# Performance work log

Hardware: AMD Instinct MI355X
Metric: run time of the kernel (lower is better)

The kernel has to match this reference:

```python
import jax, jax.numpy as jnp
import numpy as np

CUTOFF = 100.0
SR = 16000.0
Q = 0.7071067811865476  # 1/sqrt(2), torchaudio default
BATCH, T = 64, 480000


def _biquad_coeffs():
    # RBJ highpass biquad coefficients, normalized by a0
    w0 = 2.0 * np.pi * CUTOFF / SR
    alpha = np.sin(w0) / (2.0 * Q)
    cosw = np.cos(w0)
    b0 = (1.0 + cosw) / 2.0
    b1 = -(1.0 + cosw)
    b2 = b0
    a0 = 1.0 + alpha
    a1 = -2.0 * cosw
    a2 = 1.0 - alpha
    return tuple(float(c / a0) for c in (b0, b1, b2, a1, a2))


def setup_inputs() -> dict:
    key = jax.random.key(0)
    audio = jax.random.normal(key, (BATCH, T), dtype=jnp.float32)
    return {"audio": audio}


def reference(audio):
    # audio: [B, T]; order-2 IIR (Direct Form I) recurrence along time
    b0, b1, b2, a1, a2 = _biquad_coeffs()

    def step(carry, x):
        x1, x2, y1, y2 = carry  # each [B]
        y = b0 * x + b1 * x1 + b2 * x2 - a1 * y1 - a2 * y2
        return (x, x1, y, y1), y

    B = audio.shape[0]
    z = jnp.zeros((B,), audio.dtype)
    _, ys = jax.lax.scan(step, (z, z, z, z), audio.T)  # ys: [T, B]
    return ys.T
```

## Files before the change

kernel.cpp:

```cpp
#include <hip/hip_runtime.h>
#include <cmath>

#define T_LEN 480000
#define BATCH 64
#define CHUNK 128
#define WARM  320
#define NCH   ((T_LEN + CHUNK - 1) / CHUNK)
#define BLKS  32

#define STEP(xi, yo) do {                                   \
    float f_  = fmaf(b0, (xi), fmaf(b1, x1, b2 * x2));      \
    float g_  = fmaf(c2, y2, f_);                           \
    float yy_ = fmaf(c1, y1, g_);                           \
    x2 = x1; x1 = (xi);                                     \
    y2 = y1; y1 = yy_;                                      \
    (yo) = yy_;                                             \
} while (0)

__global__ __launch_bounds__(256) void highpass_kernel(
    const float* __restrict__ in, float* __restrict__ out,
    const float b0, const float b1, const float b2,
    const float c1, const float c2)
{
    const int idx = blockIdx.x * blockDim.x + threadIdx.x;
    if (idx >= BATCH * NCH) return;
    const int r = idx / NCH;
    const int c = idx - r * NCH;

    const size_t rowoff = (size_t)r * T_LEN;
    const int begin = c * CHUNK;
    int end = begin + CHUNK; if (end > T_LEN) end = T_LEN;
    int start = begin - WARM; if (start < 0) start = 0;

    const float4* __restrict__ xv = (const float4*)(in  + rowoff + start);
    float4*       __restrict__ yv = (float4*)      (out + rowoff + start);

    const int nblk = (end - start) / BLKS;
    const int wblk = (begin - start) / BLKS;

    float x1 = 0.f, x2 = 0.f, y1 = 0.f, y2 = 0.f;

    float4 cur[8], nxt[8];
#pragma unroll
    for (int i = 0; i < 8; ++i) cur[i] = xv[i];

    for (int b = 0; b < nblk; ++b) {
        if (b + 1 < nblk) {
#pragma unroll
            for (int i = 0; i < 8; ++i) nxt[i] = xv[(b + 1) * 8 + i];
        }

        float4 o[8];
#pragma unroll
        for (int i = 0; i < 8; ++i) {
            float4 v = cur[i];
            float4 q;
            STEP(v.x, q.x);
            STEP(v.y, q.y);
            STEP(v.z, q.z);
            STEP(v.w, q.w);
            o[i] = q;
        }

        if (b >= wblk) {
#pragma unroll
            for (int i = 0; i < 8; ++i) yv[b * 8 + i] = o[i];
        }

#pragma unroll
        for (int i = 0; i < 8; ++i) cur[i] = nxt[i];
    }
}

extern "C" void kernel_launch(void* const* d_in, const int* in_sizes, int n_in,
                              void* d_out, int out_size, void* d_ws, size_t ws_size,
                              hipStream_t stream) {
    const float* in  = (const float*)d_in[0];
    float*       out = (float*)d_out;

    const double Q     = 0.7071067811865476;
    const double w0    = 2.0 * M_PI * 100.0 / 16000.0;
    const double alpha = sin(w0) / (2.0 * Q);
    const double cosw  = cos(w0);
    const double b0d = (1.0 + cosw) / 2.0;
    const double b1d = -(1.0 + cosw);
    const double b2d = b0d;
    const double a0d = 1.0 + alpha;
    const double a1d = -2.0 * cosw;
    const double a2d = 1.0 - alpha;

    const float b0 = (float)(b0d / a0d);
    const float b1 = (float)(b1d / a0d);
    const float b2 = (float)(b2d / a0d);
    const float c1 = (float)(-(a1d / a0d));
    const float c2 = (float)(-(a2d / a0d));

    const int total  = BATCH * NCH;
    const int tblock = 256;
    const int grid   = (total + tblock - 1) / tblock;

    hipLaunchKernelGGL(highpass_kernel, dim3(grid), dim3(tblock), 0, stream,
                       in, out, b0, b1, b2, c1, c2);
}
```

Baseline: 267.0 us.

## Replace per-chunk warmup recurrence with block-level state propagation via matrix powers

Each thread now runs a short 64-sample chunk from zero output state. It publishes its end state to shared memory, then reconstructs its true initial state by combining the end states of the previous six threads through precomputed powers of the 2x2 feedback matrix (A^64 up to A^320). The old scheme had each thread recompute 320 warmup samples for only 128 outputs; this removes most of that redundant input reading and arithmetic. The cost is a second pass over the registers, a block barrier, and a truncated state history of about 384 samples, comparable to the previous warmup length.

```diff
diff --git a/kernel.cpp b/kernel.cpp
--- a/kernel.cpp
+++ b/kernel.cpp
@@ -3,10 +3,11 @@
 
 #define T_LEN 480000
 #define BATCH 64
-#define CHUNK 128
-#define WARM  320
-#define NCH   ((T_LEN + CHUNK - 1) / CHUNK)
-#define BLKS  32
+#define L     64
+#define WARMT 6
+#define OUTT  (256 - WARMT)
+#define SPB   (OUTT * L)
+#define BPR   (T_LEN / SPB)
 
 #define STEP(xi, yo) do {                                   \
     float f_  = fmaf(b0, (xi), fmaf(b1, x1, b2 * x2));      \
@@ -20,56 +21,78 @@
 __global__ __launch_bounds__(256) void highpass_kernel(
     const float* __restrict__ in, float* __restrict__ out,
     const float b0, const float b1, const float b2,
-    const float c1, const float c2)
+    const float c1, const float c2,
+    const float4 M1, const float4 M2, const float4 M3,
+    const float4 M4, const float4 M5)
 {
-    const int idx = blockIdx.x * blockDim.x + threadIdx.x;
-    if (idx >= BATCH * NCH) return;
-    const int r = idx / NCH;
-    const int c = idx - r * NCH;
+    const int r = blockIdx.x / BPR;
+    const int b = blockIdx.x - r * BPR;
+    const int t = threadIdx.x;
+    const size_t rowoff = (size_t)r * T_LEN;
+    const int start = b * SPB + (t - WARMT) * L;
 
-    const size_t rowoff = (size_t)r * T_LEN;
-    const int begin = c * CHUNK;
-    int end = begin + CHUNK; if (end > T_LEN) end = T_LEN;
-    int start = begin - WARM; if (start < 0) start = 0;
+    float4 v[16];
+    float pa = 0.f, pb = 0.f;
+    float xs1 = 0.f, xs2 = 0.f;
 
-    const float4* __restrict__ xv = (const float4*)(in  + rowoff + start);
-    float4*       __restrict__ yv = (float4*)      (out + rowoff + start);
+    const bool active = (start >= 0);
+    if (active) {
+        const float4* __restrict__ xv = (const float4*)(in + rowoff + start);
+#pragma unroll
+        for (int i = 0; i < 16; ++i) v[i] = xv[i];
+        if (start > 0) {
+            xs1 = in[rowoff + start - 1];
+            xs2 = in[rowoff + start - 2];
+        }
+        float x1 = xs1, x2 = xs2, y1 = 0.f, y2 = 0.f;
+#pragma unroll
+        for (int i = 0; i < 16; ++i) {
+            float d;
+            STEP(v[i].x, d); STEP(v[i].y, d); STEP(v[i].z, d); STEP(v[i].w, d);
+        }
+        pa = y1; pb = y2;
+    }
 
-    const int nblk = (end - start) / BLKS;
-    const int wblk = (begin - start) / BLKS;
+    __shared__ float2 pl[256];
+    pl[t] = make_float2(pa, pb);
+    __syncthreads();
+    if (t < WARMT) return;
 
-    float x1 = 0.f, x2 = 0.f, y1 = 0.f, y2 = 0.f;
+    const float2 q1 = pl[t - 1], q2 = pl[t - 2], q3 = pl[t - 3],
+                 q4 = pl[t - 4], q5 = pl[t - 5], q6 = pl[t - 6];
+    float Y1 = q1.x, Y2 = q1.y;
+    Y1 = fmaf(M1.x, q2.x, fmaf(M1.y, q2.y, Y1));
+    Y2 = fmaf(M1.z, q2.x, fmaf(M1.w, q2.y, Y2));
+    Y1 = fmaf(M2.x, q3.x, fmaf(M2.y, q3.y, Y1));
+    Y2 = fmaf(M2.z, q3.x, fmaf(M2.w, q3.y, Y2));
+    Y1 = fmaf(M3.x, q4.x, fmaf(M3.y, q4.y, Y1));
+    Y2 = fmaf(M3.z, q4.x, fmaf(M3.w, q4.y, Y2));
+    Y1 = fmaf(M4.x, q5.x, fmaf(M4.y, q5.y, Y1));
+    Y2 = fmaf(M4.z, q5.x, fmaf(M4.w, q5.y, Y2));
+    Y1 = fmaf(M5.x, q6.x, fmaf(M5.y, q6.y, Y1));
+    Y2 = fmaf(M5.z, q6.x, fmaf(M5.w, q6.y, Y2));
 
-    float4 cur[8], nxt[8];
+    {
+        float x1 = xs1, x2 = xs2, y1 = Y1, y2 = Y2;
 #pragma unroll
-    for (int i = 0; i < 8; ++i) cur[i] = xv[i];
+        for (int i = 0; i < 16; ++i) {
+            float4 q;
+            STEP(v[i].x, q.x); STEP(v[i].y, q.y);
+            STEP(v[i].z, q.z); STEP(v[i].w, q.w);
+            v[i] = q;
+        }
+    }
 
-    for (int b = 0; b < nblk; ++b) {
-        if (b + 1 < nblk) {
+    float4* __restrict__ yv = (float4*)(out + rowoff + start);
 #pragma unroll
-            for (int i = 0; i < 8; ++i) nxt[i] = xv[(b + 1) * 8 + i];
-        }
+    for (int i = 0; i < 16; ++i) yv[i] = v[i];
+}
 
-        float4 o[8];
-#pragma unroll
-        for (int i = 0; i < 8; ++i) {
-            float4 v = cur[i];
-            float4 q;
-            STEP(v.x, q.x);
-            STEP(v.y, q.y);
-            STEP(v.z, q.z);
-            STEP(v.w, q.w);
-            o[i] = q;
-        }
-
-        if (b >= wblk) {
-#pragma unroll
-            for (int i = 0; i < 8; ++i) yv[b * 8 + i] = o[i];
-        }
-
-#pragma unroll
-        for (int i = 0; i < 8; ++i) cur[i] = nxt[i];
-    }
+static void matmul2(const double* a, const double* bm, double* o) {
+    o[0] = a[0]*bm[0] + a[1]*bm[2];
+    o[1] = a[0]*bm[1] + a[1]*bm[3];
+    o[2] = a[2]*bm[0] + a[3]*bm[2];
+    o[3] = a[2]*bm[1] + a[3]*bm[3];
 }
 
 extern "C" void kernel_launch(void* const* d_in, const int* in_sizes, int n_in,
@@ -86,19 +109,32 @@
     const double b1d = -(1.0 + cosw);
     const double b2d = b0d;
     const double a0d = 1.0 + alpha;
-    const double a1d = -2.0 * cosw;
-    const double a2d = 1.0 - alpha;
+    const double c1d = -(-2.0 * cosw) / a0d;
+    const double c2d = -(1.0 - alpha) / a0d;
+
+    double A[4] = {c1d, c2d, 1.0, 0.0};
+    double M[4] = {A[0], A[1], A[2], A[3]};
+    for (int s = 0; s < 6; ++s) {
+        double tmp[4]; matmul2(M, M, tmp);
+        M[0]=tmp[0]; M[1]=tmp[1]; M[2]=tmp[2]; M[3]=tmp[3];
+    }
+    double P[5][4];
+    P[0][0]=M[0]; P[0][1]=M[1]; P[0][2]=M[2]; P[0][3]=M[3];
+    for (int k = 1; k < 5; ++k) matmul2(P[k-1], M, P[k]);
+
+    float4 Mv[5];
+    for (int k = 0; k < 5; ++k)
+        Mv[k] = make_float4((float)P[k][0], (float)P[k][1],
+                            (float)P[k][2], (float)P[k][3]);
 
     const float b0 = (float)(b0d / a0d);
     const float b1 = (float)(b1d / a0d);
     const float b2 = (float)(b2d / a0d);
-    const float c1 = (float)(-(a1d / a0d));
-    const float c2 = (float)(-(a2d / a0d));
+    const float c1 = (float)c1d;
+    const float c2 = (float)c2d;
 
-    const int total  = BATCH * NCH;
-    const int tblock = 256;
-    const int grid   = (total + tblock - 1) / tblock;
-
-    hipLaunchKernelGGL(highpass_kernel, dim3(grid), dim3(tblock), 0, stream,
-                       in, out, b0, b1, b2, c1, c2);
+    const int grid = BATCH * BPR;
+    hipLaunchKernelGGL(highpass_kernel, dim3(grid), dim3(256), 0, stream,
+                       in, out, b0, b1, b2, c1, c2,
+                       Mv[0], Mv[1], Mv[2], Mv[3], Mv[4]);
 }
```

Result: faster. 230.7 us (-13.6%).
